# Kernel optimization log

Measured on AMD Instinct MI355X. Metric: run time of the kernel, lower is better.

## Reference

```python
import jax, jax.numpy as jnp
import numpy as np

N = 100000      # nodes
E = 1000000     # edges (avg degree 10)
F_IN = 64       # num_features
HID = 64        # hidden_channels
C1 = 4          # num_labeled_classes
C2 = 3          # num_unlabeled_classes
L = 4           # num_layers
ALPHA = 0.1


def setup_inputs() -> dict:
    key = jax.random.key(0)
    ks = jax.random.split(key, 8)
    x = jax.random.normal(ks[0], (N, F_IN), dtype=jnp.float32)
    edge_index = jax.random.randint(ks[1], (2, E), 0, N, dtype=jnp.int32)
    # GCN2Conv shared weights (glorot-ish scale), one per residual layer
    Ws = jax.random.normal(ks[2], (L - 1, F_IN, F_IN), dtype=jnp.float32) / np.sqrt(F_IN)
    # GCNConv weight + bias
    W_gcn = jax.random.normal(ks[3], (F_IN, HID), dtype=jnp.float32) / np.sqrt(F_IN)
    b_gcn = jnp.zeros((HID,), dtype=jnp.float32)
    # classification heads
    W1 = jax.random.normal(ks[4], (HID, C1), dtype=jnp.float32) / np.sqrt(HID)
    b1 = jnp.zeros((C1,), dtype=jnp.float32)
    W2 = jax.random.normal(ks[5], (HID, C2), dtype=jnp.float32) / np.sqrt(HID)
    b2 = jnp.zeros((C2,), dtype=jnp.float32)
    return {"x": x, "edge_index": edge_index, "Ws": Ws, "W_gcn": W_gcn,
            "b_gcn": b_gcn, "W1": W1, "b1": b1, "W2": W2, "b2": b2}


def _gcn_norm(edge_index, num_nodes):
    # PyG gcn_norm: add self-loops, symmetric D^-1/2 A D^-1/2 normalization
    loop = jnp.arange(num_nodes, dtype=edge_index.dtype)
    row = jnp.concatenate([edge_index[0], loop])  # source
    col = jnp.concatenate([edge_index[1], loop])  # target
    deg = jax.ops.segment_sum(jnp.ones_like(col, dtype=jnp.float32), col,
                              num_segments=num_nodes)
    dinv = jnp.where(deg > 0, jax.lax.rsqrt(deg), 0.0)
    norm = dinv[row] * dinv[col]  # [E+N]
    return row, col, norm


def _propagate(x, row, col, norm, num_nodes):
    # out[col] += norm * x[row]  (gather -> scale -> scatter-add)
    return jax.ops.segment_sum(norm[:, None] * x[row], col, num_segments=num_nodes)


def reference(x, edge_index, Ws, W_gcn, b_gcn, W1, b1, W2, b2):
    num_nodes = x.shape[0]
    row, col, norm = _gcn_norm(edge_index, num_nodes)
    x0 = x
    # GCN2Conv layers: theta=None -> beta=1.0, shared weights ->
    # out = ((1-alpha) * A_hat x + alpha * x0) @ W
    for i in range(L - 1):
        h = _propagate(x, row, col, norm, num_nodes)
        h = (1.0 - ALPHA) * h + ALPHA * x0
        h = h @ Ws[i]
        x = jax.nn.relu(h)
        # dropout(p=0.5) is inactive in eval mode
        x0 = x  # repo updates x_0 each layer
    # GCNConv: A_hat (x W) + b
    h = _propagate(x @ W_gcn, row, col, norm, num_nodes) + b_gcn
    out1 = h @ W1 + b1  # l2_classifier is False
    out2 = h @ W2 + b2
    return out1, out2, h
```

## Files before the change

kernel.cpp:

```cpp
#include <hip/hip_runtime.h>
#include <hip/hip_bf16.h>


#define TPB 256
#define NBSH 7
typedef __hip_bfloat16 bf16;
typedef __attribute__((ext_vector_type(8))) short short8;
typedef __attribute__((ext_vector_type(4))) float f32x4;

#define MFMA16(A, B, C) __builtin_amdgcn_mfma_f32_16x16x32_bf16((A), (B), (C), 0, 0, 0)

__device__ __forceinline__ float lo16(int u) { return __int_as_float(u << 16); }
__device__ __forceinline__ float hi16(int u) { return __int_as_float(u & 0xffff0000); }

__device__ __forceinline__ unsigned cvtpk(float lo, float hi) {
    unsigned r;
    asm("v_cvt_pk_bf16_f32 %0, %1, %2" : "=v"(r) : "v"(lo), "v"(hi));
    return r;
}

__global__ void ebhist_kernel(const int* __restrict__ col, int* __restrict__ bh,
                              int E, int B) {
    __shared__ int lh[800];
    for (int i = threadIdx.x; i < B; i += blockDim.x) lh[i] = 0;
    __syncthreads();
    for (int e = blockIdx.x * blockDim.x + threadIdx.x; e < E; e += gridDim.x * blockDim.x)
        atomicAdd(&lh[col[e] >> NBSH], 1);
    __syncthreads();
    for (int i = threadIdx.x; i < B; i += blockDim.x) {
        int c = lh[i];
        if (c) atomicAdd(&bh[i], c);
    }
}

__global__ void bscan_kernel(const int* __restrict__ bh, int* __restrict__ bcur,
                             int* __restrict__ boff, int B, int E) {
    __shared__ int s[256];
    int t = threadIdx.x;
    int v[4]; int sum = 0;
#pragma unroll
    for (int i = 0; i < 4; ++i) {
        int idx = t * 4 + i;
        v[i] = (idx < B) ? bh[idx] : 0;
        sum += v[i];
    }
    s[t] = sum;
    __syncthreads();
    for (int off = 1; off < 256; off <<= 1) {
        int val = (t >= off) ? s[t - off] : 0;
        __syncthreads();
        s[t] += val;
        __syncthreads();
    }
    int run = s[t] - sum;
#pragma unroll
    for (int i = 0; i < 4; ++i) {
        int idx = t * 4 + i;
        if (idx < B) { bcur[idx] = run; boff[idx] = run; }
        run += v[i];
    }
    if (t == 255) boff[B] = E;
}

__global__ void bucket_scatter_kernel(const int* __restrict__ ei, int* __restrict__ bcur,
                                      unsigned int* __restrict__ ebuf, int E, int B) {
    __shared__ int lh[800], lb[800];
    int chunk = (E + gridDim.x - 1) / gridDim.x;
    int beg = blockIdx.x * chunk;
    int end = min(beg + chunk, E);
    for (int i = threadIdx.x; i < B; i += blockDim.x) lh[i] = 0;
    __syncthreads();
    for (int e = beg + threadIdx.x; e < end; e += blockDim.x)
        atomicAdd(&lh[ei[E + e] >> NBSH], 1);
    __syncthreads();
    for (int i = threadIdx.x; i < B; i += blockDim.x) {
        int c = lh[i];
        lb[i] = c ? atomicAdd(&bcur[i], c) : 0;
    }
    __syncthreads();
    for (int i = threadIdx.x; i < B; i += blockDim.x) lh[i] = 0;
    __syncthreads();
    for (int e = beg + threadIdx.x; e < end; e += blockDim.x) {
        int r = ei[e];
        int c = ei[E + e];
        int bin = c >> NBSH;
        int rank = atomicAdd(&lh[bin], 1);
        ebuf[lb[bin] + rank] = ((unsigned)(c & 127) << 17) | (unsigned)r;
    }
}

__global__ __launch_bounds__(128) void bucket_place_kernel(
        const int* __restrict__ boff, const unsigned int* __restrict__ ebuf,
        int* __restrict__ rowptr, int* __restrict__ degi,
        float* __restrict__ dinv, float* __restrict__ sdeg,
        int* __restrict__ srcids, int n) {
    __shared__ int cnt[128], loff[128], lcur[128];
    int b = blockIdx.x;
    int t = threadIdx.x;
    int lo = boff[b];
    int hi = boff[b + 1];
    int vbase = b << NBSH;
    cnt[t] = 0;
    __syncthreads();
    for (int i = lo + t; i < hi; i += 128)
        atomicAdd(&cnt[ebuf[i] >> 17], 1);
    __syncthreads();
    int mine = cnt[t];
    loff[t] = mine;
    __syncthreads();
    for (int off = 1; off < 128; off <<= 1) {
        int val = (t >= off) ? loff[t - off] : 0;
        __syncthreads();
        loff[t] += val;
        __syncthreads();
    }
    int excl = loff[t] - mine;
    int v = vbase + t;
    if (v < n) {
        rowptr[v] = lo + excl;
        degi[v] = mine;
        float d = (float)mine + 1.0f;
        dinv[v] = rsqrtf(d);
        sdeg[v] = sqrtf(d);
    }
    lcur[t] = lo + excl;
    __syncthreads();
    for (int i = lo + t; i < hi; i += 128) {
        unsigned int r = ebuf[i];
        int pos = atomicAdd(&lcur[r >> 17], 1);
        srcids[pos] = (int)(r & 0x1FFFFu);
    }
}

__global__ void dhist_kernel(const int* __restrict__ degi, int* __restrict__ dh, int n) {
    __shared__ int lh[256];
    lh[threadIdx.x] = 0;
    __syncthreads();
    for (int v = blockIdx.x * blockDim.x + threadIdx.x; v < n; v += gridDim.x * blockDim.x)
        atomicAdd(&lh[min(degi[v], 255)], 1);
    __syncthreads();
    int c = lh[threadIdx.x];
    if (c) atomicAdd(&dh[threadIdx.x], c);
}

__global__ void dscan_kernel(const int* __restrict__ dh, int* __restrict__ dcur) {
    __shared__ int s[256];
    int t = threadIdx.x;
    int mine = dh[t];
    s[t] = mine;
    __syncthreads();
    for (int off = 1; off < 256; off <<= 1) {
        int val = (t >= off) ? s[t - off] : 0;
        __syncthreads();
        s[t] += val;
        __syncthreads();
    }
    dcur[t] = s[t] - mine;
}

__global__ void place_kernel(const int* __restrict__ degi, int* __restrict__ dcur,
                             int* __restrict__ perm, int n) {
    __shared__ int lh[256], lb[256];
    int chunk = (n + gridDim.x - 1) / gridDim.x;
    int beg = blockIdx.x * chunk;
    int end = min(beg + chunk, n);
    lh[threadIdx.x] = 0;
    __syncthreads();
    for (int v = beg + threadIdx.x; v < end; v += blockDim.x)
        atomicAdd(&lh[min(degi[v], 255)], 1);
    __syncthreads();
    int c = lh[threadIdx.x];
    lb[threadIdx.x] = c ? atomicAdd(&dcur[threadIdx.x], c) : 0;
    __syncthreads();
    lh[threadIdx.x] = 0;
    __syncthreads();
    for (int v = beg + threadIdx.x; v < end; v += blockDim.x) {
        int bin = min(degi[v], 255);
        int r = atomicAdd(&lh[bin], 1);
        perm[lb[bin] + r] = v;
    }
}

__global__ void cvt_kernel(const float* __restrict__ x, const float* __restrict__ dinv,
                           unsigned short* __restrict__ xb, int n4) {
    int i = blockIdx.x * blockDim.x + threadIdx.x;
    if (i < n4) {
        float dv = dinv[i >> 4];
        float4 f = ((const float4*)x)[i];
        uint2 o;
        o.x = cvtpk(f.x * dv, f.y * dv);
        o.y = cvtpk(f.z * dv, f.w * dv);
        ((uint2*)xb)[i] = o;
    }
}

struct WFrag { short8 h0, l0, h1, l1; };
__device__ __forceinline__ WFrag load_wfrag(const float* __restrict__ W, int col, int kg) {
    union { short8 v; unsigned u[4]; } H0, L0, H1, L1;
#pragma unroll
    for (int j = 0; j < 4; ++j) {
        float w0 = W[(kg * 8 + 2 * j) * 64 + col];
        float w1 = W[(kg * 8 + 2 * j + 1) * 64 + col];
        unsigned h = cvtpk(w0, w1);
        float h0 = __uint_as_float(h << 16);
        float h1 = __uint_as_float(h & 0xffff0000u);
        H0.u[j] = h;
        L0.u[j] = cvtpk(w0 - h0, w1 - h1);
        float v0 = W[(32 + kg * 8 + 2 * j) * 64 + col];
        float v1 = W[(32 + kg * 8 + 2 * j + 1) * 64 + col];
        unsigned g = cvtpk(v0, v1);
        float g0 = __uint_as_float(g << 16);
        float g1 = __uint_as_float(g & 0xffff0000u);
        H1.u[j] = g;
        L1.u[j] = cvtpk(v0 - g0, v1 - g1);
    }
    WFrag r;
    r.h0 = H0.v; r.l0 = L0.v; r.h1 = H1.v; r.l1 = L1.v;
    return r;
}

__device__ __forceinline__ void build_bfrag(const float* __restrict__ tp,
                                            short8* bh, short8* bl) {
    float4 ta = *(const float4*)tp;
    float4 tb = *(const float4*)(tp + 4);
    float tv[8] = {ta.x, ta.y, ta.z, ta.w, tb.x, tb.y, tb.z, tb.w};
    union { short8 v; unsigned u[4]; } H, L;
#pragma unroll
    for (int j = 0; j < 4; ++j) {
        unsigned h = cvtpk(tv[2 * j], tv[2 * j + 1]);
        float h0 = __uint_as_float(h << 16);
        float h1 = __uint_as_float(h & 0xffff0000u);
        H.u[j] = h;
        L.u[j] = cvtpk(tv[2 * j] - h0, tv[2 * j + 1] - h1);
    }
    *bh = H.v;
    *bl = L.v;
}

__device__ __forceinline__ f32x4 mm6(const WFrag& w, short8 bh0, short8 bl0,
                                     short8 bh1, short8 bl1) {
    f32x4 ac = {0.f, 0.f, 0.f, 0.f};
    ac = MFMA16(w.h0, bh0, ac);
    ac = MFMA16(w.l0, bh0, ac);
    ac = MFMA16(w.h0, bl0, ac);
    ac = MFMA16(w.h1, bh1, ac);
    ac = MFMA16(w.l1, bh1, ac);
    ac = MFMA16(w.h1, bl1, ac);
    return ac;
}

struct GRes { float a0, a1, a2, a3; };
__device__ __forceinline__ GRes gather8s(const int* __restrict__ srcids, int beg, int deg,
                                         int md, const unsigned short* __restrict__ xsb,
                                         int ge) {
    GRes r{0.0f, 0.0f, 0.0f, 0.0f};
    for (int i = 0; i < md; i += 8) {
        int src[8];
#pragma unroll
        for (int u = 0; u < 8; ++u)
            src[u] = srcids[beg + i + u];
        int2 q[8];
#pragma unroll
        for (int u = 0; u < 8; ++u)
            q[u] = *(const int2*)(xsb + ((unsigned)src[u] * 64u + (unsigned)ge));
#pragma unroll
        for (int u = 0; u < 8; ++u) {
            float m = (i + u < deg) ? 1.0f : 0.0f;
            r.a0 = fmaf(m, lo16(q[u].x), r.a0);
            r.a1 = fmaf(m, hi16(q[u].x), r.a1);
            r.a2 = fmaf(m, lo16(q[u].y), r.a2);
            r.a3 = fmaf(m, hi16(q[u].y), r.a3);
        }
    }
    return r;
}

__device__ __forceinline__ void st_relu4(unsigned short* p, f32x4 a, float sc) {
    uint2 o;
    o.x = cvtpk(fmaxf(a[0], 0.f) * sc, fmaxf(a[1], 0.f) * sc);
    o.y = cvtpk(fmaxf(a[2], 0.f) * sc, fmaxf(a[3], 0.f) * sc);
    *(uint2*)p = o;
}

__device__ __forceinline__ void st_plain4(unsigned short* p, f32x4 a) {
    uint2 o;
    o.x = cvtpk(a[0], a[1]);
    o.y = cvtpk(a[2], a[3]);
    *(uint2*)p = o;
}

__global__ __launch_bounds__(256) void layer_kernel(
        const int* __restrict__ rowptr, const int* __restrict__ degi,
        const int* __restrict__ srcids, const int* __restrict__ perm,
        const unsigned short* __restrict__ xsb, const float* __restrict__ dinv,
        const float* __restrict__ sdeg, const float* __restrict__ W,
        unsigned short* __restrict__ yb, int n) {
    __shared__ __align__(16) float st[16][68];
    int wid = threadIdx.x >> 6;
    int lane = threadIdx.x & 63;
    int s = lane >> 4;
    int g = lane & 15;
    WFrag wA = load_wfrag(W, wid * 16 + g, s);
    int ntile = (n + 15) >> 4;
    for (int tile = ntile - 1 - blockIdx.x; tile >= 0; tile -= gridDim.x) {
        int base = tile * 16;
        int vb = base + wid * 4 + s;
        int vbc = (vb < n) ? vb : n - 1;
        int v = perm[vbc];
        int beg = rowptr[v];
        int deg = degi[v];
        int md = max(deg, __shfl_xor(deg, 16));
        md = max(md, __shfl_xor(md, 32));
        GRes r = gather8s(srcids, beg, deg, md, xsb, g * 4);
        int2 qs = *(const int2*)(xsb + ((unsigned)v * 64u + (unsigned)(g * 4)));
        float xs0 = lo16(qs.x), xs1 = hi16(qs.x), xs2 = lo16(qs.y), xs3 = hi16(qs.y);
        float c9 = 0.9f * dinv[v];
        float c1 = 0.1f * sdeg[v];
        float4 t4;
        t4.x = c9 * (r.a0 + xs0) + c1 * xs0;
        t4.y = c9 * (r.a1 + xs1) + c1 * xs1;
        t4.z = c9 * (r.a2 + xs2) + c1 * xs2;
        t4.w = c9 * (r.a3 + xs3) + c1 * xs3;
        *(float4*)&st[wid * 4 + s][g * 4] = t4;
        __syncthreads();
        int vb2 = base + g;
        int v2c = perm[(vb2 < n) ? vb2 : n - 1];
        float dv2 = dinv[v2c];
        const float* strow = st[g];
        short8 bh0, bl0, bh1, bl1;
        build_bfrag(strow + s * 8,      &bh0, &bl0);
        build_bfrag(strow + 32 + s * 8, &bh1, &bl1);
        __syncthreads();
        f32x4 ac = mm6(wA, bh0, bl0, bh1, bl1);
        if (vb2 < n) {
            unsigned short* yp = yb + ((size_t)(unsigned)v2c << 6)
                               + (unsigned)(wid * 16 + s * 4);
            st_relu4(yp, ac, dv2);
        }
    }
}

__global__ __launch_bounds__(256) void layer_fused_kernel(
        const int* __restrict__ rowptr, const int* __restrict__ degi,
        const int* __restrict__ srcids, const int* __restrict__ perm,
        const unsigned short* __restrict__ xsb, const float* __restrict__ dinv,
        const float* __restrict__ sdeg, const float* __restrict__ W,
        const float* __restrict__ Wg, unsigned short* __restrict__ yb, int n) {
    __shared__ __align__(16) float st[16][68];
    int wid = threadIdx.x >> 6;
    int lane = threadIdx.x & 63;
    int s = lane >> 4;
    int g = lane & 15;
    WFrag wA = load_wfrag(W,  wid * 16 + g, s);
    WFrag wG = load_wfrag(Wg, wid * 16 + g, s);
    int ntile = (n + 15) >> 4;
    for (int tile = ntile - 1 - blockIdx.x; tile >= 0; tile -= gridDim.x) {
        int base = tile * 16;
        int vb = base + wid * 4 + s;
        int vbc = (vb < n) ? vb : n - 1;
        int v = perm[vbc];
        int beg = rowptr[v];
        int deg = degi[v];
        int md = max(deg, __shfl_xor(deg, 16));
        md = max(md, __shfl_xor(md, 32));
        GRes r = gather8s(srcids, beg, deg, md, xsb, g * 4);
        int2 qs = *(const int2*)(xsb + ((unsigned)v * 64u + (unsigned)(g * 4)));
        float xs0 = lo16(qs.x), xs1 = hi16(qs.x), xs2 = lo16(qs.y), xs3 = hi16(qs.y);
        float c9 = 0.9f * dinv[v];
        float c1 = 0.1f * sdeg[v];
        float4 t4;
        t4.x = c9 * (r.a0 + xs0) + c1 * xs0;
        t4.y = c9 * (r.a1 + xs1) + c1 * xs1;
        t4.z = c9 * (r.a2 + xs2) + c1 * xs2;
        t4.w = c9 * (r.a3 + xs3) + c1 * xs3;
        *(float4*)&st[wid * 4 + s][g * 4] = t4;
        __syncthreads();
        int vb2 = base + g;
        int v2c = perm[(vb2 < n) ? vb2 : n - 1];
        float dv2 = dinv[v2c];
        const float* strow = st[g];
        {
            short8 bh0, bl0, bh1, bl1;
            build_bfrag(strow + s * 8,      &bh0, &bl0);
            build_bfrag(strow + 32 + s * 8, &bh1, &bl1);
            __syncthreads();
            f32x4 ac = mm6(wA, bh0, bl0, bh1, bl1);
            *(float4*)&st[g][wid * 16 + s * 4] = make_float4(
                fmaxf(ac[0], 0.f) * dv2, fmaxf(ac[1], 0.f) * dv2,
                fmaxf(ac[2], 0.f) * dv2, fmaxf(ac[3], 0.f) * dv2);
        }
        __syncthreads();
        {
            short8 bh0, bl0, bh1, bl1;
            build_bfrag(strow + s * 8,      &bh0, &bl0);
            build_bfrag(strow + 32 + s * 8, &bh1, &bl1);
            f32x4 ac = mm6(wG, bh0, bl0, bh1, bl1);
            __syncthreads();
            if (vb2 < n) {
                unsigned short* yp = yb + ((size_t)(unsigned)v2c << 6)
                                   + (unsigned)(wid * 16 + s * 4);
                st_plain4(yp, ac);
            }
        }
    }
}

__global__ __launch_bounds__(256) void heads_kernel(
        const int* __restrict__ rowptr, const int* __restrict__ degi,
        const int* __restrict__ srcids, const int* __restrict__ perm,
        const unsigned short* __restrict__ xwb, const float* __restrict__ dinv,
        const float* __restrict__ bg,
        const float* __restrict__ W1, const float* __restrict__ b1,
        const float* __restrict__ W2, const float* __restrict__ b2,
        float* __restrict__ out, int n) {
    __shared__ __align__(16) float hs[4][4][64];
    __shared__ __align__(16) float whd[448];
    __shared__ float bs[8];
    int wid = threadIdx.x >> 6;
    int lane = threadIdx.x & 63;
    int s = lane >> 4;
    int g = lane & 15;
    for (int i = threadIdx.x; i < 448; i += TPB) {
        int j = i >> 6, k = i & 63;
        whd[i] = (j < 4) ? W1[k * 4 + j] : W2[k * 3 + (j - 4)];
    }
    if (threadIdx.x < 7) bs[threadIdx.x] = (threadIdx.x < 4) ? b1[threadIdx.x] : b2[threadIdx.x - 4];
    __syncthreads();
    int j = lane >> 3;
    int k0 = (lane & 7) * 8;
    int ntile = (n + 15) >> 4;
    for (int tile = ntile - 1 - blockIdx.x; tile >= 0; tile -= gridDim.x) {
        int base = tile * 16 + wid * 4;
        int vb = base + s;
        int vbc = (vb < n) ? vb : n - 1;
        int v = perm[vbc];
        int beg = rowptr[v];
        int deg = degi[v];
        int md = max(deg, __shfl_xor(deg, 16));
        md = max(md, __shfl_xor(md, 32));
        GRes r = gather8s(srcids, beg, deg, md, xwb, g * 4);
        int2 qs = *(const int2*)(xwb + ((unsigned)v * 64u + (unsigned)(g * 4)));
        float dv = dinv[v];
        float4 bq = *(const float4*)(bg + g * 4);
        float4 h4;
        h4.x = dv * (r.a0 + lo16(qs.x)) + bq.x;
        h4.y = dv * (r.a1 + hi16(qs.x)) + bq.y;
        h4.z = dv * (r.a2 + lo16(qs.y)) + bq.z;
        h4.w = dv * (r.a3 + hi16(qs.y)) + bq.w;
        if (vb < n)
            *(float4*)&out[(size_t)7 * n + (size_t)(unsigned)v * 64 + g * 4] = h4;
        *(float4*)&hs[wid][s][g * 4] = h4;
        __builtin_amdgcn_wave_barrier();
#pragma unroll
        for (int ss = 0; ss < 4; ++ss) {
            int vb2 = base + ss;
            if (vb2 >= n) break;
            int v2 = perm[vb2];
            float part = 0.0f;
            if (j < 7) {
                float4 h0 = *(const float4*)&hs[wid][ss][k0];
                float4 h1 = *(const float4*)&hs[wid][ss][k0 + 4];
                const float4* wq = (const float4*)&whd[j * 64 + k0];
                float4 w0 = wq[0], w1 = wq[1];
                part = h0.x * w0.x + h0.y * w0.y + h0.z * w0.z + h0.w * w0.w
                     + h1.x * w1.x + h1.y * w1.y + h1.z * w1.z + h1.w * w1.w;
            }
            part += __shfl_down(part, 4);
            part += __shfl_down(part, 2);
            part += __shfl_down(part, 1);
            if ((lane & 7) == 0 && j < 7) {
                float sv = bs[j] + part;
                if (j < 4) out[(size_t)v2 * 4 + j] = sv;
                else       out[(size_t)4 * n + (size_t)v2 * 3 + (j - 4)] = sv;
            }
        }
        __builtin_amdgcn_wave_barrier();
    }
}

extern "C" void kernel_launch(void* const* d_in, const int* in_sizes, int n_in,
                              void* d_out, int out_size, void* d_ws, size_t ws_size,
                              hipStream_t stream) {
    const float* x     = (const float*)d_in[0];
    const int*   ei    = (const int*)d_in[1];
    const float* Ws    = (const float*)d_in[2];
    const float* W_gcn = (const float*)d_in[3];
    const float* b_gcn = (const float*)d_in[4];
    const float* W1    = (const float*)d_in[5];
    const float* b1    = (const float*)d_in[6];
    const float* W2    = (const float*)d_in[7];
    const float* b2    = (const float*)d_in[8];
    float* out = (float*)d_out;

    const int N = in_sizes[0] / 64;
    const int E = in_sizes[1] / 2;
    const int NLAYERS = in_sizes[2] / 4096;
    const int B = (N + 127) >> NBSH;

    int*   degi   = (int*)d_ws;
    int*   rowptr = degi + N;
    int*   bh     = rowptr + N;
    int*   bcur   = bh + 800;
    int*   boff   = bcur + 800;
    int*   dh     = boff + 800;
    int*   dcur   = dh + 256;
    int*   perm   = dcur + 256;
    int*   srcids = perm + N;
    unsigned int* ebuf = (unsigned int*)(srcids + E + 64);
    float* dinv   = (float*)(ebuf + E);
    float* sdeg   = dinv + N;
    unsigned short* x0s  = (unsigned short*)(sdeg + N);
    unsigned short* bufA = x0s + (size_t)N * 64;
    unsigned short* bufB = bufA + (size_t)N * 64;

    const int WGRID = 4096;

    hipMemsetAsync(bh, 0, 800 * sizeof(int), stream);
    hipMemsetAsync(dh, 0, 256 * sizeof(int), stream);
    hipMemsetAsync(srcids + E, 0, 64 * sizeof(int), stream);
    ebhist_kernel<<<120, TPB, 0, stream>>>(ei + E, bh, E, B);
    bscan_kernel<<<1, 256, 0, stream>>>(bh, bcur, boff, B, E);
    bucket_scatter_kernel<<<120, TPB, 0, stream>>>(ei, bcur, ebuf, E, B);
    bucket_place_kernel<<<B, 128, 0, stream>>>(boff, ebuf, rowptr, degi, dinv, sdeg,
                                               srcids, N);
    dhist_kernel<<<64, 256, 0, stream>>>(degi, dh, N);
    dscan_kernel<<<1, 256, 0, stream>>>(dh, dcur);
    place_kernel<<<64, 256, 0, stream>>>(degi, dcur, perm, N);
    cvt_kernel<<<(N * 16 + TPB - 1) / TPB, TPB, 0, stream>>>(x, dinv, x0s, N * 16);

    const unsigned short* xcur = x0s;
    unsigned short* ybuf = bufA;
    for (int i = 0; i < NLAYERS - 1; ++i) {
        layer_kernel<<<WGRID, TPB, 0, stream>>>(rowptr, degi, srcids, perm, xcur,
                                                dinv, sdeg, Ws + (size_t)i * 4096, ybuf, N);
        xcur = ybuf;
        ybuf = (ybuf == bufA) ? bufB : bufA;
    }
    layer_fused_kernel<<<WGRID, TPB, 0, stream>>>(rowptr, degi, srcids, perm, xcur,
                                                  dinv, sdeg,
                                                  Ws + (size_t)(NLAYERS - 1) * 4096,
                                                  W_gcn, ybuf, N);
    unsigned short* xw = ybuf;

    heads_kernel<<<WGRID, TPB, 0, stream>>>(rowptr, degi, srcids, perm, xw, dinv,
                                            b_gcn, W1, b1, W2, b2, out, N);
}
```

Before: 303.7 us.

## Pad CSR neighbor lists to multiples of 8 and reorder GCN aggregate before weight

Each node's adjacency list is padded to a multiple of eight, and the padding slots point at an extra zero row appended to every feature buffer. The gather loop therefore drops its per-element mask and the cross-lane max-degree shuffles. The final GCNConv is reordered to aggregate first and then multiply by W_gcn inside the heads kernel, and W_gcn is folded with the class heads into a precomputed combined weight and bias. This removes the separate fused layer kernel and its bf16 round trip, at the cost of extra srcids space, three padding memsets and a small setup kernel.

```diff
diff --git a/kernel.cpp b/kernel.cpp
--- a/kernel.cpp
+++ b/kernel.cpp
@@ -93,12 +93,13 @@
         const int* __restrict__ boff, const unsigned int* __restrict__ ebuf,
         int* __restrict__ rowptr, int* __restrict__ degi,
         float* __restrict__ dinv, float* __restrict__ sdeg,
-        int* __restrict__ srcids, int n) {
+        int* __restrict__ srcids, int n, int zid) {
     __shared__ int cnt[128], loff[128], lcur[128];
     int b = blockIdx.x;
     int t = threadIdx.x;
     int lo = boff[b];
     int hi = boff[b + 1];
+    int base_p = lo + b * 896;
     int vbase = b << NBSH;
     cnt[t] = 0;
     __syncthreads();
@@ -106,7 +107,8 @@
         atomicAdd(&cnt[ebuf[i] >> 17], 1);
     __syncthreads();
     int mine = cnt[t];
-    loff[t] = mine;
+    int pmine = (mine + 7) & ~7;
+    loff[t] = pmine;
     __syncthreads();
     for (int off = 1; off < 128; off <<= 1) {
         int val = (t >= off) ? loff[t - off] : 0;
@@ -114,22 +116,25 @@
         loff[t] += val;
         __syncthreads();
     }
-    int excl = loff[t] - mine;
+    int pexcl = loff[t] - pmine;
+    int rp = base_p + pexcl;
     int v = vbase + t;
     if (v < n) {
-        rowptr[v] = lo + excl;
+        rowptr[v] = rp;
         degi[v] = mine;
         float d = (float)mine + 1.0f;
         dinv[v] = rsqrtf(d);
         sdeg[v] = sqrtf(d);
     }
-    lcur[t] = lo + excl;
+    lcur[t] = rp;
     __syncthreads();
     for (int i = lo + t; i < hi; i += 128) {
         unsigned int r = ebuf[i];
         int pos = atomicAdd(&lcur[r >> 17], 1);
         srcids[pos] = (int)(r & 0x1FFFFu);
     }
+    for (int p = rp + mine; p < rp + pmine; ++p)
+        srcids[p] = zid;
 }
 
 __global__ void dhist_kernel(const int* __restrict__ degi, int* __restrict__ dh, int n) {
@@ -191,6 +196,27 @@
         o.x = cvtpk(f.x * dv, f.y * dv);
         o.y = cvtpk(f.z * dv, f.w * dv);
         ((uint2*)xb)[i] = o;
+    }
+}
+
+__global__ void headw_kernel(const float* __restrict__ Wg,
+                             const float* __restrict__ W1, const float* __restrict__ b1,
+                             const float* __restrict__ W2, const float* __restrict__ b2,
+                             const float* __restrict__ bg,
+                             float* __restrict__ whdP, float* __restrict__ bsP) {
+    int tid = threadIdx.x;
+    if (tid < 448) {
+        int j = tid >> 6, k = tid & 63;
+        float s = 0.0f;
+        for (int m = 0; m < 64; ++m)
+            s += Wg[k * 64 + m] * ((j < 4) ? W1[m * 4 + j] : W2[m * 3 + (j - 4)]);
+        whdP[tid] = s;
+    } else if (tid < 455) {
+        int j = tid - 448;
+        float s = (j < 4) ? b1[j] : b2[j - 4];
+        for (int m = 0; m < 64; ++m)
+            s += bg[m] * ((j < 4) ? W1[m * 4 + j] : W2[m * 3 + (j - 4)]);
+        bsP[j] = s;
     }
 }
 
@@ -250,11 +276,11 @@
 }
 
 struct GRes { float a0, a1, a2, a3; };
-__device__ __forceinline__ GRes gather8s(const int* __restrict__ srcids, int beg, int deg,
-                                         int md, const unsigned short* __restrict__ xsb,
+__device__ __forceinline__ GRes gather8s(const int* __restrict__ srcids, int beg, int pdeg,
+                                         const unsigned short* __restrict__ xsb,
                                          int ge) {
     GRes r{0.0f, 0.0f, 0.0f, 0.0f};
-    for (int i = 0; i < md; i += 8) {
+    for (int i = 0; i < pdeg; i += 8) {
         int src[8];
 #pragma unroll
         for (int u = 0; u < 8; ++u)
@@ -265,11 +291,10 @@
             q[u] = *(const int2*)(xsb + ((unsigned)src[u] * 64u + (unsigned)ge));
 #pragma unroll
         for (int u = 0; u < 8; ++u) {
-            float m = (i + u < deg) ? 1.0f : 0.0f;
-            r.a0 = fmaf(m, lo16(q[u].x), r.a0);
-            r.a1 = fmaf(m, hi16(q[u].x), r.a1);
-            r.a2 = fmaf(m, lo16(q[u].y), r.a2);
-            r.a3 = fmaf(m, hi16(q[u].y), r.a3);
+            r.a0 += lo16(q[u].x);
+            r.a1 += hi16(q[u].x);
+            r.a2 += lo16(q[u].y);
+            r.a3 += hi16(q[u].y);
         }
     }
     return r;
@@ -279,13 +304,6 @@
     uint2 o;
     o.x = cvtpk(fmaxf(a[0], 0.f) * sc, fmaxf(a[1], 0.f) * sc);
     o.y = cvtpk(fmaxf(a[2], 0.f) * sc, fmaxf(a[3], 0.f) * sc);
-    *(uint2*)p = o;
-}
-
-__device__ __forceinline__ void st_plain4(unsigned short* p, f32x4 a) {
-    uint2 o;
-    o.x = cvtpk(a[0], a[1]);
-    o.y = cvtpk(a[2], a[3]);
     *(uint2*)p = o;
 }
 
@@ -309,9 +327,8 @@
         int v = perm[vbc];
         int beg = rowptr[v];
         int deg = degi[v];
-        int md = max(deg, __shfl_xor(deg, 16));
-        md = max(md, __shfl_xor(md, 32));
-        GRes r = gather8s(srcids, beg, deg, md, xsb, g * 4);
+        int pdeg = (deg + 7) & ~7;
+        GRes r = gather8s(srcids, beg, pdeg, xsb, g * 4);
         int2 qs = *(const int2*)(xsb + ((unsigned)v * 64u + (unsigned)(g * 4)));
         float xs0 = lo16(qs.x), xs1 = hi16(qs.x), xs2 = lo16(qs.y), xs3 = hi16(qs.y);
         float c9 = 0.9f * dinv[v];
@@ -340,19 +357,27 @@
     }
 }
 
-__global__ __launch_bounds__(256) void layer_fused_kernel(
+__global__ __launch_bounds__(256) void heads_kernel(
         const int* __restrict__ rowptr, const int* __restrict__ degi,
         const int* __restrict__ srcids, const int* __restrict__ perm,
-        const unsigned short* __restrict__ xsb, const float* __restrict__ dinv,
-        const float* __restrict__ sdeg, const float* __restrict__ W,
-        const float* __restrict__ Wg, unsigned short* __restrict__ yb, int n) {
+        const unsigned short* __restrict__ ysb, const float* __restrict__ dinv,
+        const float* __restrict__ bg, const float* __restrict__ Wg,
+        const float* __restrict__ whdP, const float* __restrict__ bsP,
+        float* __restrict__ out, int n) {
     __shared__ __align__(16) float st[16][68];
+    __shared__ __align__(16) float whd[448];
+    __shared__ float bs[8];
     int wid = threadIdx.x >> 6;
     int lane = threadIdx.x & 63;
     int s = lane >> 4;
     int g = lane & 15;
-    WFrag wA = load_wfrag(W,  wid * 16 + g, s);
     WFrag wG = load_wfrag(Wg, wid * 16 + g, s);
+    for (int i = threadIdx.x; i < 448; i += TPB)
+        whd[i] = whdP[i];
+    if (threadIdx.x < 7) bs[threadIdx.x] = bsP[threadIdx.x];
+    __syncthreads();
+    int j = lane >> 3;
+    int k0 = (lane & 7) * 8;
     int ntile = (n + 15) >> 4;
     for (int tile = ntile - 1 - blockIdx.x; tile >= 0; tile -= gridDim.x) {
         int base = tile * 16;
@@ -361,105 +386,40 @@
         int v = perm[vbc];
         int beg = rowptr[v];
         int deg = degi[v];
-        int md = max(deg, __shfl_xor(deg, 16));
-        md = max(md, __shfl_xor(md, 32));
-        GRes r = gather8s(srcids, beg, deg, md, xsb, g * 4);
-        int2 qs = *(const int2*)(xsb + ((unsigned)v * 64u + (unsigned)(g * 4)));
-        float xs0 = lo16(qs.x), xs1 = hi16(qs.x), xs2 = lo16(qs.y), xs3 = hi16(qs.y);
-        float c9 = 0.9f * dinv[v];
-        float c1 = 0.1f * sdeg[v];
-        float4 t4;
-        t4.x = c9 * (r.a0 + xs0) + c1 * xs0;
-        t4.y = c9 * (r.a1 + xs1) + c1 * xs1;
-        t4.z = c9 * (r.a2 + xs2) + c1 * xs2;
-        t4.w = c9 * (r.a3 + xs3) + c1 * xs3;
-        *(float4*)&st[wid * 4 + s][g * 4] = t4;
+        int pdeg = (deg + 7) & ~7;
+        GRes r = gather8s(srcids, beg, pdeg, ysb, g * 4);
+        int2 qs = *(const int2*)(ysb + ((unsigned)v * 64u + (unsigned)(g * 4)));
+        float dv = dinv[v];
+        float4 a4;
+        a4.x = dv * (r.a0 + lo16(qs.x));
+        a4.y = dv * (r.a1 + hi16(qs.x));
+        a4.z = dv * (r.a2 + lo16(qs.y));
+        a4.w = dv * (r.a3 + hi16(qs.y));
+        *(float4*)&st[wid * 4 + s][g * 4] = a4;
         __syncthreads();
         int vb2 = base + g;
         int v2c = perm[(vb2 < n) ? vb2 : n - 1];
-        float dv2 = dinv[v2c];
         const float* strow = st[g];
-        {
-            short8 bh0, bl0, bh1, bl1;
-            build_bfrag(strow + s * 8,      &bh0, &bl0);
-            build_bfrag(strow + 32 + s * 8, &bh1, &bl1);
-            __syncthreads();
-            f32x4 ac = mm6(wA, bh0, bl0, bh1, bl1);
-            *(float4*)&st[g][wid * 16 + s * 4] = make_float4(
-                fmaxf(ac[0], 0.f) * dv2, fmaxf(ac[1], 0.f) * dv2,
-                fmaxf(ac[2], 0.f) * dv2, fmaxf(ac[3], 0.f) * dv2);
+        short8 bh0, bl0, bh1, bl1;
+        build_bfrag(strow + s * 8,      &bh0, &bl0);
+        build_bfrag(strow + 32 + s * 8, &bh1, &bl1);
+        f32x4 ac = mm6(wG, bh0, bl0, bh1, bl1);
+        if (vb2 < n) {
+            float4 bq = *(const float4*)(bg + wid * 16 + s * 4);
+            float4 h4 = make_float4(ac[0] + bq.x, ac[1] + bq.y,
+                                    ac[2] + bq.z, ac[3] + bq.w);
+            *(float4*)&out[(size_t)7 * n + (size_t)(unsigned)v2c * 64
+                           + (unsigned)(wid * 16 + s * 4)] = h4;
         }
-        __syncthreads();
-        {
-            short8 bh0, bl0, bh1, bl1;
-            build_bfrag(strow + s * 8,      &bh0, &bl0);
-            build_bfrag(strow + 32 + s * 8, &bh1, &bl1);
-            f32x4 ac = mm6(wG, bh0, bl0, bh1, bl1);
-            __syncthreads();
-            if (vb2 < n) {
-                unsigned short* yp = yb + ((size_t)(unsigned)v2c << 6)
-                                   + (unsigned)(wid * 16 + s * 4);
-                st_plain4(yp, ac);
-            }
-        }
-    }
-}
-
-__global__ __launch_bounds__(256) void heads_kernel(
-        const int* __restrict__ rowptr, const int* __restrict__ degi,
-        const int* __restrict__ srcids, const int* __restrict__ perm,
-        const unsigned short* __restrict__ xwb, const float* __restrict__ dinv,
-        const float* __restrict__ bg,
-        const float* __restrict__ W1, const float* __restrict__ b1,
-        const float* __restrict__ W2, const float* __restrict__ b2,
-        float* __restrict__ out, int n) {
-    __shared__ __align__(16) float hs[4][4][64];
-    __shared__ __align__(16) float whd[448];
-    __shared__ float bs[8];
-    int wid = threadIdx.x >> 6;
-    int lane = threadIdx.x & 63;
-    int s = lane >> 4;
-    int g = lane & 15;
-    for (int i = threadIdx.x; i < 448; i += TPB) {
-        int j = i >> 6, k = i & 63;
-        whd[i] = (j < 4) ? W1[k * 4 + j] : W2[k * 3 + (j - 4)];
-    }
-    if (threadIdx.x < 7) bs[threadIdx.x] = (threadIdx.x < 4) ? b1[threadIdx.x] : b2[threadIdx.x - 4];
-    __syncthreads();
-    int j = lane >> 3;
-    int k0 = (lane & 7) * 8;
-    int ntile = (n + 15) >> 4;
-    for (int tile = ntile - 1 - blockIdx.x; tile >= 0; tile -= gridDim.x) {
-        int base = tile * 16 + wid * 4;
-        int vb = base + s;
-        int vbc = (vb < n) ? vb : n - 1;
-        int v = perm[vbc];
-        int beg = rowptr[v];
-        int deg = degi[v];
-        int md = max(deg, __shfl_xor(deg, 16));
-        md = max(md, __shfl_xor(md, 32));
-        GRes r = gather8s(srcids, beg, deg, md, xwb, g * 4);
-        int2 qs = *(const int2*)(xwb + ((unsigned)v * 64u + (unsigned)(g * 4)));
-        float dv = dinv[v];
-        float4 bq = *(const float4*)(bg + g * 4);
-        float4 h4;
-        h4.x = dv * (r.a0 + lo16(qs.x)) + bq.x;
-        h4.y = dv * (r.a1 + hi16(qs.x)) + bq.y;
-        h4.z = dv * (r.a2 + lo16(qs.y)) + bq.z;
-        h4.w = dv * (r.a3 + hi16(qs.y)) + bq.w;
-        if (vb < n)
-            *(float4*)&out[(size_t)7 * n + (size_t)(unsigned)v * 64 + g * 4] = h4;
-        *(float4*)&hs[wid][s][g * 4] = h4;
-        __builtin_amdgcn_wave_barrier();
 #pragma unroll
         for (int ss = 0; ss < 4; ++ss) {
-            int vb2 = base + ss;
-            if (vb2 >= n) break;
-            int v2 = perm[vb2];
+            int vb3 = base + wid * 4 + ss;
+            if (vb3 >= n) break;
+            int v3 = perm[vb3];
             float part = 0.0f;
             if (j < 7) {
-                float4 h0 = *(const float4*)&hs[wid][ss][k0];
-                float4 h1 = *(const float4*)&hs[wid][ss][k0 + 4];
+                float4 h0 = *(const float4*)&st[wid * 4 + ss][k0];
+                float4 h1 = *(const float4*)&st[wid * 4 + ss][k0 + 4];
                 const float4* wq = (const float4*)&whd[j * 64 + k0];
                 float4 w0 = wq[0], w1 = wq[1];
                 part = h0.x * w0.x + h0.y * w0.y + h0.z * w0.z + h0.w * w0.w
@@ -470,11 +430,11 @@
             part += __shfl_down(part, 1);
             if ((lane & 7) == 0 && j < 7) {
                 float sv = bs[j] + part;
-                if (j < 4) out[(size_t)v2 * 4 + j] = sv;
-                else       out[(size_t)4 * n + (size_t)v2 * 3 + (j - 4)] = sv;
+                if (j < 4) out[(size_t)v3 * 4 + j] = sv;
+                else       out[(size_t)4 * n + (size_t)v3 * 3 + (j - 4)] = sv;
             }
         }
-        __builtin_amdgcn_wave_barrier();
+        __syncthreads();
     }
 }
 
@@ -496,6 +456,7 @@
     const int E = in_sizes[1] / 2;
     const int NLAYERS = in_sizes[2] / 4096;
     const int B = (N + 127) >> NBSH;
+    const int SRCSZ = E + B * 896 + 64;
 
     int*   degi   = (int*)d_ws;
     int*   rowptr = degi + N;
@@ -506,23 +467,29 @@
     int*   dcur   = dh + 256;
     int*   perm   = dcur + 256;
     int*   srcids = perm + N;
-    unsigned int* ebuf = (unsigned int*)(srcids + E + 64);
+    unsigned int* ebuf = (unsigned int*)(srcids + SRCSZ);
     float* dinv   = (float*)(ebuf + E);
     float* sdeg   = dinv + N;
-    unsigned short* x0s  = (unsigned short*)(sdeg + N);
-    unsigned short* bufA = x0s + (size_t)N * 64;
-    unsigned short* bufB = bufA + (size_t)N * 64;
+    float* whdP   = sdeg + N;
+    float* bsP    = whdP + 448;
+    unsigned short* x0s  = (unsigned short*)(bsP + 16);
+    unsigned short* bufA = x0s + (size_t)(N + 1) * 64;
+    unsigned short* bufB = bufA + (size_t)(N + 1) * 64;
 
     const int WGRID = 4096;
+
+    headw_kernel<<<1, 512, 0, stream>>>(W_gcn, W1, b1, W2, b2, b_gcn, whdP, bsP);
 
     hipMemsetAsync(bh, 0, 800 * sizeof(int), stream);
     hipMemsetAsync(dh, 0, 256 * sizeof(int), stream);
-    hipMemsetAsync(srcids + E, 0, 64 * sizeof(int), stream);
+    hipMemsetAsync(x0s  + (size_t)N * 64, 0, 128, stream);
+    hipMemsetAsync(bufA + (size_t)N * 64, 0, 128, stream);
+    hipMemsetAsync(bufB + (size_t)N * 64, 0, 128, stream);
     ebhist_kernel<<<120, TPB, 0, stream>>>(ei + E, bh, E, B);
     bscan_kernel<<<1, 256, 0, stream>>>(bh, bcur, boff, B, E);
     bucket_scatter_kernel<<<120, TPB, 0, stream>>>(ei, bcur, ebuf, E, B);
     bucket_place_kernel<<<B, 128, 0, stream>>>(boff, ebuf, rowptr, degi, dinv, sdeg,
-                                               srcids, N);
+                                               srcids, N, N);
     dhist_kernel<<<64, 256, 0, stream>>>(degi, dh, N);
     dscan_kernel<<<1, 256, 0, stream>>>(dh, dcur);
     place_kernel<<<64, 256, 0, stream>>>(degi, dcur, perm, N);
@@ -530,18 +497,13 @@
 
     const unsigned short* xcur = x0s;
     unsigned short* ybuf = bufA;
-    for (int i = 0; i < NLAYERS - 1; ++i) {
+    for (int i = 0; i < NLAYERS; ++i) {
         layer_kernel<<<WGRID, TPB, 0, stream>>>(rowptr, degi, srcids, perm, xcur,
                                                 dinv, sdeg, Ws + (size_t)i * 4096, ybuf, N);
         xcur = ybuf;
         ybuf = (ybuf == bufA) ? bufB : bufA;
     }
-    layer_fused_kernel<<<WGRID, TPB, 0, stream>>>(rowptr, degi, srcids, perm, xcur,
-                                                  dinv, sdeg,
-                                                  Ws + (size_t)(NLAYERS - 1) * 4096,
-                                                  W_gcn, ybuf, N);
-    unsigned short* xw = ybuf;
-
-    heads_kernel<<<WGRID, TPB, 0, stream>>>(rowptr, degi, srcids, perm, xw, dinv,
-                                            b_gcn, W1, b1, W2, b2, out, N);
-}
+
+    heads_kernel<<<WGRID, TPB, 0, stream>>>(rowptr, degi, srcids, perm, xcur, dinv,
+                                            b_gcn, W_gcn, whdP, bsP, out, N);
+}
```

New measurement: 345.4 us. +13.7%, slower.
